# Optimization experiments

Measured on AMD Instinct MI355X. Metric: run time of the kernel, lower is better.

Reference implementation:

```python
import jax, jax.numpy as jnp
import numpy as np

GAMMA, ZETA = -0.1, 1.1
N_BITS = 4
QMAX = (1 << N_BITS) - 1  # 15
OUT, IN, D, K = 4096, 4096, 8, 4096
L = (OUT * IN) // D  # 2097152 blocks, no padding needed


def setup_inputs() -> dict:
    key = jax.random.key(0)
    k = jax.random.split(key, 7)
    x = jax.random.normal(k[0], (4, 2048, IN), jnp.float32)
    codebook = jax.random.normal(k[1], (K, D), jnp.float32)
    indices = jax.random.randint(k[2], (L,), 0, K, jnp.int32)
    base_int = jax.random.randint(k[3], (OUT, IN), 0, QMAX, jnp.int32)
    scale = jax.random.uniform(k[4], (OUT, 1), jnp.float32)
    zero = jax.random.uniform(k[5], (OUT, 1), jnp.float32)
    bias = jax.random.normal(k[6], (OUT,), jnp.float32)
    return {"x": x, "codebook": codebook, "indices": indices,
            "base_int": base_int, "scale": scale, "zero": zero, "bias": bias}


def reference(x, codebook, indices, base_int, scale, zero, bias):
    # Gather codebook blocks and rebuild alpha with the weight's shape [OUT, IN]
    alpha = codebook[indices].reshape(OUT, IN)
    # Rectified sigmoid (soft quant mode)
    r = jnp.clip(jax.nn.sigmoid(alpha) * (ZETA - GAMMA) + GAMMA, 0.0, 1.0)
    # Affine int-quant reconstruction
    q_int = jnp.clip(base_int.astype(scale.dtype) + r + zero, 0.0, float(QMAX))
    Wq = scale * (q_int - zero)  # [OUT, IN]
    # F.linear: x @ Wq^T + bias
    return jnp.einsum('bsi,oi->bso', x, Wq) + bias
```

## Files before the change

### kernel.cpp

```cpp
#include <hip/hip_runtime.h>

#define M_DIM 8192
#define N_DIM 4096
#define K_DIM 4096
#define L_BLK 2097152
#define K2 8192

typedef __attribute__((ext_vector_type(8))) short short8;
typedef __attribute__((ext_vector_type(8))) unsigned short ushort8;
typedef __attribute__((ext_vector_type(16))) float f32x16;

__device__ __forceinline__ unsigned short f2bf(float f) {
  unsigned int u = __float_as_uint(f);
  unsigned int r = (u + 0x7fffu + ((u >> 16) & 1u)) >> 16;
  return (unsigned short)r;
}

__device__ __forceinline__ void gld16(const void* g, void* l) {
  __builtin_amdgcn_global_load_lds(
      (const __attribute__((address_space(1))) void*)g,
      (__attribute__((address_space(3))) void*)l, 16, 0, 0);
}

__global__ void prep_kernel(const float* __restrict__ cb,
                            const int* __restrict__ idx,
                            const int* __restrict__ base,
                            const float* __restrict__ scale,
                            const float* __restrict__ zero,
                            const float* __restrict__ x,
                            unsigned short* __restrict__ W,
                            unsigned short* __restrict__ xb) {
  if (blockIdx.x < L_BLK / 256) {
    const int b = blockIdx.x * 256 + threadIdx.x;
    const int o = b >> 9;
    const float s = scale[o];
    const float z = zero[o];
    const int ci = idx[b];
    const float4* crow = (const float4*)(cb + (size_t)ci * 8);
    float4 c0 = crow[0], c1 = crow[1];
    const int4* brow = (const int4*)(base + (size_t)b * 8);
    int4 b0 = brow[0], b1 = brow[1];
    float a[8]  = {c0.x, c0.y, c0.z, c0.w, c1.x, c1.y, c1.z, c1.w};
    int   bi[8] = {b0.x, b0.y, b0.z, b0.w, b1.x, b1.y, b1.z, b1.w};
    union { unsigned short h[8]; ushort8 v; } u;
#pragma unroll
    for (int d = 0; d < 8; ++d) {
      float sg = 1.0f / (1.0f + __expf(-a[d]));
      float r = fminf(fmaxf(sg * 1.2f - 0.1f, 0.0f), 1.0f);
      float q = fminf(fmaxf((float)bi[d] + r + z, 0.0f), 15.0f);
      u.h[d] = f2bf(s * (q - z));
    }
    *(ushort8*)(W + (size_t)b * 8) = u.v;
  } else {
    const size_t i = (size_t)(blockIdx.x - L_BLK / 256) * 256 + threadIdx.x;
    const float4* X = (const float4*)x;
    float4 a0 = X[i * 2], a1 = X[i * 2 + 1];
    float f[8] = {a0.x, a0.y, a0.z, a0.w, a1.x, a1.y, a1.z, a1.w};
    union { unsigned short h[8]; ushort8 v; } u;
#pragma unroll
    for (int d = 0; d < 8; ++d) u.h[d] = f2bf(f[d]);
    *(ushort8*)(xb + i * 8) = u.v;
  }
}


#define VMW(N) asm volatile("s_waitcnt vmcnt(" #N ")" ::: "memory")
#define BAR __builtin_amdgcn_s_barrier()

#define RDB32(BUFO) \
  _Pragma("unroll") for (int nf = 0; nf < 2; ++nf) \
  _Pragma("unroll") for (int ks = 0; ks < 4; ++ks) \
    bf[nf][ks] = *(const short8*)(lds + (BUFO) + 32768 + \
        (wn * 64 + nf * 32 + l31) * 128 + ((ks * 32 + h16) ^ swz));

#define RDA32(BUFO, MF) \
  _Pragma("unroll") for (int ks = 0; ks < 4; ++ks) \
    af[ks] = *(const short8*)(lds + (BUFO) + \
        (wm * 128 + (MF) * 32 + l31) * 128 + ((ks * 32 + h16) ^ swz));

#define FM32(MF) do { \
  __builtin_amdgcn_s_setprio(1); \
  _Pragma("unroll") for (int ks = 0; ks < 4; ++ks) \
  _Pragma("unroll") for (int nf = 0; nf < 2; ++nf) \
    acc[MF][nf] = __builtin_amdgcn_mfma_f32_32x32x16_bf16( \
        af[ks], bf[nf][ks], acc[MF][nf], 0, 0, 0); \
  __builtin_amdgcn_s_setprio(0); \
} while (0)

#define ITER(CUR, NXT, T) do { \
   RDB32(CUR); RDA32(CUR, 0); \
  stA(NXT, 1, (T) + 1); stA(NXT, 3, (T) + 1); \
  BAR; FM32(0); BAR; \
   RDA32(CUR, 1); \
  stB(CUR, 0, (T) + 2); stB(CUR, 1, (T) + 2); \
  BAR; FM32(1); BAR; \
   RDA32(CUR, 2); \
  stB(CUR, 2, (T) + 2); stB(CUR, 3, (T) + 2); \
  BAR; FM32(2); BAR; \
   RDA32(CUR, 3); \
  stA(CUR, 0, (T) + 2); stA(CUR, 2, (T) + 2); \
  VMW(6); BAR; FM32(3); BAR; \
} while (0)

__global__ __launch_bounds__(512, 2)
void gemm_bt(const unsigned short* __restrict__ A,
             const unsigned short* __restrict__ B,
             const float* __restrict__ bias,
             float* __restrict__ C) {
  __shared__ char lds[131072];
  const int tid = threadIdx.x;
  const int lane = tid & 63;
  const int w = tid >> 6;
  const int wm = w >> 2;
  const int wn = w & 3;
  const int l31 = lane & 31;
  const int h16 = (lane >> 5) * 16;
  const int swz = (l31 & 7) << 4;

  const int s = (int)blockIdx.x;
  const int wg = (s & 7) * 64 + (s >> 3);
  const int bm = wg & 31;
  const int bn = wg >> 5;

  const char* Abase = (const char*)A + (size_t)bm * 256 * K2;
  const char* Bbase = (const char*)B + (size_t)bn * 256 * K2;

  const int strow = tid >> 3;
  const int scol = ((tid & 7) * 16) ^ ((strow & 7) << 4);
  const int sdst = w * 1024;

  auto stA = [&](int bo, int c, int kt) {
    gld16(Abase + (size_t)(c * 64 + strow) * K2 + kt * 128 + scol,
          lds + bo + c * 8192 + sdst);
  };
  auto stB = [&](int bo, int c, int kt) {
    gld16(Bbase + (size_t)(c * 64 + strow) * K2 + kt * 128 + scol,
          lds + bo + 32768 + c * 8192 + sdst);
  };

  f32x16 acc[4][2] = {};
  short8 bf[2][4];
  short8 af[4];

  stB(0, 0, 0); stB(0, 1, 0); stB(0, 2, 0); stB(0, 3, 0);
  stA(0, 0, 0); stA(0, 1, 0); stA(0, 2, 0); stA(0, 3, 0);
  stB(65536, 0, 1); stB(65536, 1, 1); stB(65536, 2, 1); stB(65536, 3, 1);
  stA(65536, 0, 1); stA(65536, 2, 1);
  VMW(6); BAR;

  for (int tp = 0; tp < 31; ++tp) {
    ITER(0, 65536, 2 * tp);
    ITER(65536, 0, 2 * tp + 1);
  }
  RDB32(0); RDA32(0, 0);
  stA(65536, 1, 63); stA(65536, 3, 63);
  BAR; FM32(0); BAR;
  RDA32(0, 1);
  BAR; FM32(1); BAR;
  RDA32(0, 2);
  BAR; FM32(2); BAR;
  RDA32(0, 3);
  VMW(0); BAR; FM32(3); BAR;
  RDB32(65536); RDA32(65536, 0);
  FM32(0);
  RDA32(65536, 1);
  FM32(1);
  RDA32(65536, 2);
  FM32(2);
  RDA32(65536, 3);
  FM32(3);

  const int cb0 = bn * 256 + wn * 64 + l31;
  const int h4 = (lane >> 5) * 4;
  float bv0 = bias[cb0];
  float bv1 = bias[cb0 + 32];
#pragma unroll
  for (int mf = 0; mf < 4; ++mf) {
#pragma unroll
    for (int r = 0; r < 16; ++r) {
      int row = bm * 256 + wm * 128 + mf * 32 + (r & 3) + 8 * (r >> 2) + h4;
      float* Crow = C + (size_t)row * N_DIM + cb0;
      Crow[0]  = acc[mf][0][r] + bv0;
      Crow[32] = acc[mf][1][r] + bv1;
    }
  }
}

extern "C" void kernel_launch(void* const* d_in, const int* in_sizes, int n_in,
                              void* d_out, int out_size, void* d_ws, size_t ws_size,
                              hipStream_t stream) {
  const float* x     = (const float*)d_in[0];
  const float* cb    = (const float*)d_in[1];
  const int*   idx   = (const int*)d_in[2];
  const int*   base  = (const int*)d_in[3];
  const float* scale = (const float*)d_in[4];
  const float* zero  = (const float*)d_in[5];
  const float* bias  = (const float*)d_in[6];
  float* out = (float*)d_out;

  unsigned short* Wq = (unsigned short*)d_ws;
  unsigned short* Xb = (unsigned short*)((char*)d_ws + (size_t)N_DIM * K_DIM * 2);

  const int prep_blocks = L_BLK / 256 + (M_DIM * K_DIM / 8) / 256;
  prep_kernel<<<prep_blocks, 256, 0, stream>>>(cb, idx, base, scale, zero, x, Wq, Xb);
  gemm_bt<<<(M_DIM / 256) * (N_DIM / 256), 512, 0, stream>>>(Xb, Wq, bias, out);
}
```

Baseline: 328.9 us.

## Use K-chunk-major LDS layout, reorder loads, remap tiles, grid-stride prep

The GEMM's LDS tiles move from a swizzled row-major layout to one where each 16-byte k-chunk is a separate 4 KB plane, so each thread loads one row's chunk and fragment reads become contiguous per lane. The prefetch schedule now issues all four A chunks for the next tile before the B chunks, and the vmcnt waits are adjusted to match. Workgroups are remapped so each XCD covers an 8x8 block of output tiles, aiming for better L2 reuse. The prep kernel becomes a grid-stride loop over 2048 blocks, which cuts launch and scheduling overhead but gives each thread more serial work.

New measurement: 398.7 us. +21.2%, slower.

```diff
diff --git a/kernel.cpp b/kernel.cpp
--- a/kernel.cpp
+++ b/kernel.cpp
@@ -21,6 +21,8 @@
       (const __attribute__((address_space(1))) void*)g,
       (__attribute__((address_space(3))) void*)l, 16, 0, 0);
 }
+
+#define PREP_THREADS (2048 * 256)
 
 __global__ void prep_kernel(const float* __restrict__ cb,
                             const int* __restrict__ idx,
@@ -30,36 +32,41 @@
                             const float* __restrict__ x,
                             unsigned short* __restrict__ W,
                             unsigned short* __restrict__ xb) {
-  if (blockIdx.x < L_BLK / 256) {
-    const int b = blockIdx.x * 256 + threadIdx.x;
-    const int o = b >> 9;
-    const float s = scale[o];
-    const float z = zero[o];
-    const int ci = idx[b];
-    const float4* crow = (const float4*)(cb + (size_t)ci * 8);
-    float4 c0 = crow[0], c1 = crow[1];
-    const int4* brow = (const int4*)(base + (size_t)b * 8);
-    int4 b0 = brow[0], b1 = brow[1];
-    float a[8]  = {c0.x, c0.y, c0.z, c0.w, c1.x, c1.y, c1.z, c1.w};
-    int   bi[8] = {b0.x, b0.y, b0.z, b0.w, b1.x, b1.y, b1.z, b1.w};
-    union { unsigned short h[8]; ushort8 v; } u;
-#pragma unroll
-    for (int d = 0; d < 8; ++d) {
-      float sg = 1.0f / (1.0f + __expf(-a[d]));
-      float r = fminf(fmaxf(sg * 1.2f - 0.1f, 0.0f), 1.0f);
-      float q = fminf(fmaxf((float)bi[d] + r + z, 0.0f), 15.0f);
-      u.h[d] = f2bf(s * (q - z));
+  const int tid0 = blockIdx.x * 256 + threadIdx.x;
+#pragma unroll 1
+  for (long long i = tid0; i < (long long)L_BLK + (long long)M_DIM * K_DIM / 8;
+       i += PREP_THREADS) {
+    if (i < L_BLK) {
+      const int b = (int)i;
+      const int o = b >> 9;
+      const float s = scale[o];
+      const float z = zero[o];
+      const int ci = idx[b];
+      const float4* crow = (const float4*)(cb + (size_t)ci * 8);
+      float4 c0 = crow[0], c1 = crow[1];
+      const int4* brow = (const int4*)(base + (size_t)b * 8);
+      int4 b0 = brow[0], b1 = brow[1];
+      float a[8]  = {c0.x, c0.y, c0.z, c0.w, c1.x, c1.y, c1.z, c1.w};
+      int   bi[8] = {b0.x, b0.y, b0.z, b0.w, b1.x, b1.y, b1.z, b1.w};
+      union { unsigned short h[8]; ushort8 v; } u;
+#pragma unroll
+      for (int d = 0; d < 8; ++d) {
+        float sg = 1.0f / (1.0f + __expf(-a[d]));
+        float r = fminf(fmaxf(sg * 1.2f - 0.1f, 0.0f), 1.0f);
+        float q = fminf(fmaxf((float)bi[d] + r + z, 0.0f), 15.0f);
+        u.h[d] = f2bf(s * (q - z));
+      }
+      *(ushort8*)(W + (size_t)b * 8) = u.v;
+    } else {
+      const size_t j = (size_t)(i - L_BLK);
+      const float4* X = (const float4*)x;
+      float4 a0 = X[j * 2], a1 = X[j * 2 + 1];
+      float f[8] = {a0.x, a0.y, a0.z, a0.w, a1.x, a1.y, a1.z, a1.w};
+      union { unsigned short h[8]; ushort8 v; } u;
+#pragma unroll
+      for (int d = 0; d < 8; ++d) u.h[d] = f2bf(f[d]);
+      *(ushort8*)(xb + j * 8) = u.v;
     }
-    *(ushort8*)(W + (size_t)b * 8) = u.v;
-  } else {
-    const size_t i = (size_t)(blockIdx.x - L_BLK / 256) * 256 + threadIdx.x;
-    const float4* X = (const float4*)x;
-    float4 a0 = X[i * 2], a1 = X[i * 2 + 1];
-    float f[8] = {a0.x, a0.y, a0.z, a0.w, a1.x, a1.y, a1.z, a1.w};
-    union { unsigned short h[8]; ushort8 v; } u;
-#pragma unroll
-    for (int d = 0; d < 8; ++d) u.h[d] = f2bf(f[d]);
-    *(ushort8*)(xb + i * 8) = u.v;
   }
 }
 
@@ -71,12 +78,12 @@
   _Pragma("unroll") for (int nf = 0; nf < 2; ++nf) \
   _Pragma("unroll") for (int ks = 0; ks < 4; ++ks) \
     bf[nf][ks] = *(const short8*)(lds + (BUFO) + 32768 + \
-        (wn * 64 + nf * 32 + l31) * 128 + ((ks * 32 + h16) ^ swz));
+        (ks * 2 + h) * 4096 + (wn * 64 + nf * 32 + l31) * 16);
 
 #define RDA32(BUFO, MF) \
   _Pragma("unroll") for (int ks = 0; ks < 4; ++ks) \
     af[ks] = *(const short8*)(lds + (BUFO) + \
-        (wm * 128 + (MF) * 32 + l31) * 128 + ((ks * 32 + h16) ^ swz));
+        (ks * 2 + h) * 4096 + (wm * 128 + (MF) * 32 + l31) * 16);
 
 #define FM32(MF) do { \
   __builtin_amdgcn_s_setprio(1); \
@@ -89,17 +96,17 @@
 
 #define ITER(CUR, NXT, T) do { \
    RDB32(CUR); RDA32(CUR, 0); \
-  stA(NXT, 1, (T) + 1); stA(NXT, 3, (T) + 1); \
+  stA(NXT, 0, (T) + 1); stA(NXT, 1, (T) + 1); \
   BAR; FM32(0); BAR; \
    RDA32(CUR, 1); \
-  stB(CUR, 0, (T) + 2); stB(CUR, 1, (T) + 2); \
+  stA(NXT, 2, (T) + 1); stA(NXT, 3, (T) + 1); \
   BAR; FM32(1); BAR; \
    RDA32(CUR, 2); \
-  stB(CUR, 2, (T) + 2); stB(CUR, 3, (T) + 2); \
+  stB(CUR, 0, (T) + 2); stB(CUR, 1, (T) + 2); \
   BAR; FM32(2); BAR; \
    RDA32(CUR, 3); \
-  stA(CUR, 0, (T) + 2); stA(CUR, 2, (T) + 2); \
-  VMW(6); BAR; FM32(3); BAR; \
+  stB(CUR, 2, (T) + 2); stB(CUR, 3, (T) + 2); \
+  VMW(4); BAR; FM32(3); BAR; \
 } while (0)
 
 __global__ __launch_bounds__(512, 2)
@@ -114,27 +121,27 @@
   const int wm = w >> 2;
   const int wn = w & 3;
   const int l31 = lane & 31;
-  const int h16 = (lane >> 5) * 16;
-  const int swz = (l31 & 7) << 4;
+  const int h = lane >> 5;
 
   const int s = (int)blockIdx.x;
-  const int wg = (s & 7) * 64 + (s >> 3);
-  const int bm = wg & 31;
-  const int bn = wg >> 5;
+  const int xcd = s & 7;
+  const int l = s >> 3;
+  const int bm = (xcd & 3) * 8 + (l & 7);
+  const int bn = (xcd >> 2) * 8 + (l >> 3);
 
   const char* Abase = (const char*)A + (size_t)bm * 256 * K2;
   const char* Bbase = (const char*)B + (size_t)bn * 256 * K2;
 
-  const int strow = tid >> 3;
-  const int scol = ((tid & 7) * 16) ^ ((strow & 7) << 4);
+  const int srow = tid & 255;
+  const int skh = tid >> 8;
   const int sdst = w * 1024;
 
   auto stA = [&](int bo, int c, int kt) {
-    gld16(Abase + (size_t)(c * 64 + strow) * K2 + kt * 128 + scol,
+    gld16(Abase + (size_t)srow * K2 + kt * 128 + (2 * c + skh) * 16,
           lds + bo + c * 8192 + sdst);
   };
   auto stB = [&](int bo, int c, int kt) {
-    gld16(Bbase + (size_t)(c * 64 + strow) * K2 + kt * 128 + scol,
+    gld16(Bbase + (size_t)srow * K2 + kt * 128 + (2 * c + skh) * 16,
           lds + bo + 32768 + c * 8192 + sdst);
   };
 
@@ -145,17 +152,17 @@
   stB(0, 0, 0); stB(0, 1, 0); stB(0, 2, 0); stB(0, 3, 0);
   stA(0, 0, 0); stA(0, 1, 0); stA(0, 2, 0); stA(0, 3, 0);
   stB(65536, 0, 1); stB(65536, 1, 1); stB(65536, 2, 1); stB(65536, 3, 1);
-  stA(65536, 0, 1); stA(65536, 2, 1);
-  VMW(6); BAR;
+  VMW(4); BAR;
 
   for (int tp = 0; tp < 31; ++tp) {
     ITER(0, 65536, 2 * tp);
     ITER(65536, 0, 2 * tp + 1);
   }
   RDB32(0); RDA32(0, 0);
-  stA(65536, 1, 63); stA(65536, 3, 63);
+  stA(65536, 0, 63); stA(65536, 1, 63);
   BAR; FM32(0); BAR;
   RDA32(0, 1);
+  stA(65536, 2, 63); stA(65536, 3, 63);
   BAR; FM32(1); BAR;
   RDA32(0, 2);
   BAR; FM32(2); BAR;
@@ -171,7 +178,7 @@
   FM32(3);
 
   const int cb0 = bn * 256 + wn * 64 + l31;
-  const int h4 = (lane >> 5) * 4;
+  const int h4 = h * 4;
   float bv0 = bias[cb0];
   float bv1 = bias[cb0 + 32];
 #pragma unroll
@@ -201,7 +208,6 @@
   unsigned short* Wq = (unsigned short*)d_ws;
   unsigned short* Xb = (unsigned short*)((char*)d_ws + (size_t)N_DIM * K_DIM * 2);
 
-  const int prep_blocks = L_BLK / 256 + (M_DIM * K_DIM / 8) / 256;
-  prep_kernel<<<prep_blocks, 256, 0, stream>>>(cb, idx, base, scale, zero, x, Wq, Xb);
+  prep_kernel<<<2048, 256, 0, stream>>>(cb, idx, base, scale, zero, x, Wq, Xb);
   gemm_bt<<<(M_DIM / 256) * (N_DIM / 256), 512, 0, stream>>>(Xb, Wq, bias, out);
 }
```
